# Optimization experiments

Hardware: AMD Instinct MI355X
Metric: run time of the kernel (lower is better)

## Reference

```python
import jax, jax.numpy as jnp
import numpy as np

N = 100000      # nodes per graph-batch
E = 1600000     # edges per graph-batch (avg degree 16)
G = 64          # graphs per batch (segments for mean pool)
DIN = 128
DH = 128


def setup_inputs() -> dict:
    key = jax.random.key(0)
    ks = jax.random.split(key, 14)
    x0 = jax.random.normal(ks[0], (N, DIN), jnp.float32)
    x1 = jax.random.normal(ks[1], (N, DIN), jnp.float32)
    edge_index0 = jax.random.randint(ks[2], (2, E), 0, N)
    edge_index1 = jax.random.randint(ks[3], (2, E), 0, N)
    batch0 = jnp.sort(jax.random.randint(ks[4], (N,), 0, G))
    batch1 = jnp.sort(jax.random.randint(ks[5], (N,), 0, G))
    s = 0.05
    W1 = jax.random.normal(ks[6], (DIN, DH), jnp.float32) * s
    b1 = jnp.zeros((DH,), jnp.float32)
    W2 = jax.random.normal(ks[7], (DH, DH), jnp.float32) * s
    b2 = jnp.zeros((DH,), jnp.float32)
    Wc1 = jax.random.normal(ks[8], (2 * DH, DH), jnp.float32) * s
    bc1 = jnp.zeros((DH,), jnp.float32)
    Wc2 = jax.random.normal(ks[9], (DH, 1), jnp.float32) * s
    bc2 = jnp.zeros((1,), jnp.float32)
    return dict(x0=x0, x1=x1, edge_index0=edge_index0, edge_index1=edge_index1,
                batch0=batch0, batch1=batch1,
                W1=W1, b1=b1, W2=W2, b2=b2, Wc1=Wc1, bc1=bc1, Wc2=Wc2, bc2=bc2)


def gcn_conv(x, edge_index, W, b):
    # PyG GCNConv: add self-loops, symmetric norm D^-1/2 (A+I) D^-1/2, then XW + b
    n = x.shape[0]
    sl = jnp.arange(n)
    src = jnp.concatenate([edge_index[0], sl])
    dst = jnp.concatenate([edge_index[1], sl])
    ones = jnp.ones(src.shape[0], x.dtype)
    deg = jax.ops.segment_sum(ones, dst, num_segments=n)
    dinv = jnp.where(deg > 0, jax.lax.rsqrt(deg), 0.0)
    norm = dinv[src] * dinv[dst]               # [E+N]
    h = x @ W                                   # [N, DH]
    msg = h[src] * norm[:, None]                # gather + scale
    return jax.ops.segment_sum(msg, dst, num_segments=n) + b


def graph_embedding(x, edge_index, batch, W1, b1, W2, b2):
    f = gcn_conv(x, edge_index, W1, b1)
    # dropout is identity in eval mode
    f = gcn_conv(f, edge_index, W2, b2)
    s = jax.ops.segment_sum(f, batch, num_segments=G)
    cnt = jax.ops.segment_sum(jnp.ones((f.shape[0],), f.dtype), batch, num_segments=G)
    return s / jnp.maximum(cnt, 1.0)[:, None]   # global_mean_pool -> [G, DH]


def reference(x0, x1, edge_index0, edge_index1, batch0, batch1,
              W1, b1, W2, b2, Wc1, bc1, Wc2, bc2):
    f0 = graph_embedding(x0, edge_index0, batch0, W1, b1, W2, b2)
    f1 = graph_embedding(x1, edge_index1, batch1, W1, b1, W2, b2)
    c = jnp.concatenate([f0, f1], axis=1)       # [G, 2*DH]
    h = jax.nn.sigmoid(c @ Wc1 + bc1)
    prob = jax.nn.sigmoid(h @ Wc2 + bc2)
    return prob[:, 0]                           # squeeze(-1) -> [G]
```

## Files before the change

kernel.cpp:

```cpp
#include <hip/hip_runtime.h>
#include <hip/hip_bf16.h>

#define NN 100000
#define NE 1600000
#define NG 64
#define DHID 128
#define PB 32
#define NBUCK 196
#define CAPE 10240
#define CHUNK 8192

#if __has_builtin(__builtin_amdgcn_cvt_pk_f32_fp8) && __has_builtin(__builtin_amdgcn_cvt_pk_fp8_f32)
#define FP8_HW 1
#endif

typedef float f32x2 __attribute__((ext_vector_type(2)));
typedef float f32x4 __attribute__((ext_vector_type(4)));
typedef short bf16x8 __attribute__((ext_vector_type(8)));

__device__ __forceinline__ float fp8_dec_sw(unsigned b) {
    unsigned u = ((b & 0x80u) << 24) | ((b & 0x7fu) << 20);
    return __uint_as_float(u) * 0x1p+120f;
}
__device__ __forceinline__ unsigned fp8_enc_sw(float f) {
    unsigned s = (__float_as_uint(f) >> 24) & 0x80u;
    float af = fabsf(f);
    if (!(af > 0x1p-10f)) return s;
    if (af > 448.f) af = 448.f;
    int e; float m = frexpf(af, &e);
    int ee = e + 6;
    unsigned bits;
    if (ee <= 0) {
        int k = (int)rintf(af * 512.0f);
        if (k > 7) k = 7;
        bits = (unsigned)k;
    } else {
        int mm = (int)rintf(m * 16.0f);
        if (mm == 16) { mm = 8; ee += 1; }
        if (ee > 15) { ee = 15; mm = 14; }
        bits = ((unsigned)ee << 3) | (unsigned)(mm - 8);
    }
    return s | bits;
}

__device__ __forceinline__ unsigned short fp8_pack2(float a, float b) {
#ifdef FP8_HW
    return (unsigned short)__builtin_amdgcn_cvt_pk_fp8_f32(a, b, 0, false);
#else
    return (unsigned short)(fp8_enc_sw(a) | (fp8_enc_sw(b) << 8));
#endif
}

__device__ __forceinline__ void fp8_acc4(unsigned u, float& a0, float& a1, float& a2, float& a3) {
#ifdef FP8_HW
    f32x2 lo = __builtin_amdgcn_cvt_pk_f32_fp8((int)u, false);
    f32x2 hi = __builtin_amdgcn_cvt_pk_f32_fp8((int)u, true);
    a0 += lo[0]; a1 += lo[1]; a2 += hi[0]; a3 += hi[1];
#else
    a0 += fp8_dec_sw(u & 0xffu);
    a1 += fp8_dec_sw((u >> 8) & 0xffu);
    a2 += fp8_dec_sw((u >> 16) & 0xffu);
    a3 += fp8_dec_sw(u >> 24);
#endif
}

__device__ __forceinline__ unsigned short f2bf(float f) {
    unsigned u = __float_as_uint(f);
    return (unsigned short)((u + 0x7FFFu + ((u >> 16) & 1u)) >> 16);
}


__global__ void initcur_kernel(int* __restrict__ cursor) {
    int t = threadIdx.x;
    if (t < NBUCK) cursor[t] = t * CAPE;
}

__global__ __launch_bounds__(256) void bin_kernel(const int* __restrict__ ei, int* __restrict__ cursor,
                                                  unsigned int* __restrict__ binned, int E) {
    __shared__ int hist[256], scn[256], lofs[256], lcur[256], basex[256];
    __shared__ unsigned int stage[CHUNK];
    __shared__ unsigned char stageB[CHUNK];
    int t = threadIdx.x;
    int c0 = blockIdx.x * CHUNK;
    int cend = min(c0 + CHUNK, E);
    hist[t] = 0;
    __syncthreads();
    for (int e = c0 + t; e < cend; e += 256)
        atomicAdd(&hist[((unsigned)ei[E + e]) >> 9], 1);
    __syncthreads();
    scn[t] = hist[t];
    __syncthreads();
    for (int off = 1; off < 256; off <<= 1) {
        int v = (t >= off) ? scn[t - off] : 0;
        __syncthreads();
        scn[t] += v;
        __syncthreads();
    }
    int excl = scn[t] - hist[t];
    lofs[t] = excl;
    lcur[t] = excl;
    if (hist[t] > 0) basex[t] = atomicAdd(&cursor[t], hist[t]);
    __syncthreads();
    for (int e = c0 + t; e < cend; e += 256) {
        int dst = ei[E + e], src = ei[e];
        int b = ((unsigned)dst) >> 9;
        int r = atomicAdd(&lcur[b], 1);
        stage[r]  = (((unsigned)(dst & 511)) << 17) | (unsigned)src;
        stageB[r] = (unsigned char)b;
    }
    __syncthreads();
    int cnt = cend - c0;
    for (int i = t; i < cnt; i += 256) {
        int b = stageB[i];
        binned[basex[b] + (i - lofs[b])] = stage[i];
    }
}

__global__ __launch_bounds__(256) void fine_kernel(const int* __restrict__ cursor,
                                                   unsigned int* __restrict__ binned,
                                                   float* __restrict__ dinv, int2* __restrict__ rng) {
    __shared__ unsigned int stage[CAPE];
    __shared__ int hist[512], ofs[512], lcur[512];
    __shared__ int pscan[256];
    int b = blockIdx.x, t = threadIdx.x;
    int gbase = b * CAPE;
    int cnt = min(cursor[b] - gbase, CAPE);
    for (int i = t; i < cnt; i += 256) stage[i] = binned[gbase + i];
    hist[t] = 0; hist[t + 256] = 0;
    __syncthreads();
    for (int i = t; i < cnt; i += 256) atomicAdd(&hist[stage[i] >> 17], 1);
    __syncthreads();
    int a0 = hist[2 * t], a1 = hist[2 * t + 1];
    pscan[t] = a0 + a1;
    __syncthreads();
    for (int off = 1; off < 256; off <<= 1) {
        int v = (t >= off) ? pscan[t - off] : 0;
        __syncthreads();
        pscan[t] += v;
        __syncthreads();
    }
    int pex = pscan[t] - (a0 + a1);
    ofs[2 * t] = pex;       ofs[2 * t + 1] = pex + a0;
    lcur[2 * t] = pex;      lcur[2 * t + 1] = pex + a0;
    __syncthreads();
#pragma unroll
    for (int q = 0; q < 2; ++q) {
        int l = t + 256 * q;
        int node = b * 512 + l;
        if (node < NN) {
            int dg = hist[l];
            dinv[node] = rsqrtf((float)(dg + 1));
            rng[node] = make_int2(gbase + ofs[l], gbase + ofs[l] + dg);
        }
    }
    for (int i = t; i < cnt; i += 256) {
        unsigned int p = stage[i];
        int l = p >> 17;
        int r = atomicAdd(&lcur[l], 1);
        binned[gbase + r] = p & 0x1FFFFu;
    }
}


__global__ void bounds_kernel(const int* __restrict__ b0, const int* __restrict__ b1,
                              int* __restrict__ bounds, int n) {
    int t = threadIdx.x;
    int gb = t >> 6, j = t & 63;
    const int* b = gb ? b1 : b0;
    int lo = 0, hi = n;
    while (lo < hi) { int mid = (lo + hi) >> 1; if (b[mid] < j) lo = mid + 1; else hi = mid; }
    bounds[gb * 65 + j] = lo;
    if (j == 0) bounds[gb * 65 + 64] = n;
}


__global__ __launch_bounds__(256) void wpack_kernel(const float* __restrict__ W, unsigned short* __restrict__ Wp) {
    for (int o = blockIdx.x * 256 + threadIdx.x; o < 128 * 128; o += 2048) {
        int j = o & 7, l = (o >> 3) & 63, tile = o >> 9;
        int kt = tile >> 3, ct = tile & 7;
        int k = kt * 32 + ((l >> 4) << 3) + j;
        int c = ct * 16 + (l & 15);
        Wp[o] = f2bf(W[k * 128 + c]);
    }
}


template<bool BF16IN>
__global__ __launch_bounds__(256) void gemm_mfma(const void* __restrict__ Avoid,
                                                 const unsigned short* __restrict__ Wp,
                                                 const float* __restrict__ dinv,
                                                 unsigned int* __restrict__ Hs8dw, int n) {
    int wave = threadIdx.x >> 6, lane = threadIdx.x & 63;
    int row_base = blockIdx.x * 64 + wave * 16;
    int r = lane & 15, kg = lane >> 4;
    int rowc = min(row_base + r, n - 1);

    bf16x8 af[4];
    if (BF16IN) {
        const uint4* A = (const uint4*)Avoid;
#pragma unroll
        for (int kt = 0; kt < 4; ++kt) {
            uint4 p = A[(size_t)rowc * 16 + kt * 4 + kg];
            af[kt] = *(bf16x8*)&p;
        }
    } else {
        const float4* A = (const float4*)Avoid;
#pragma unroll
        for (int kt = 0; kt < 4; ++kt) {
            float4 p0 = A[(size_t)rowc * 32 + kt * 8 + kg * 2];
            float4 p1 = A[(size_t)rowc * 32 + kt * 8 + kg * 2 + 1];
            bf16x8 a;
            a[0] = (short)f2bf(p0.x); a[1] = (short)f2bf(p0.y);
            a[2] = (short)f2bf(p0.z); a[3] = (short)f2bf(p0.w);
            a[4] = (short)f2bf(p1.x); a[5] = (short)f2bf(p1.y);
            a[6] = (short)f2bf(p1.z); a[7] = (short)f2bf(p1.w);
            af[kt] = a;
        }
    }

    f32x4 acc[8] = {};
    const bf16x8* Wf = (const bf16x8*)Wp;
#pragma unroll
    for (int kt = 0; kt < 4; ++kt) {
#pragma unroll
        for (int ct = 0; ct < 8; ++ct) {
            bf16x8 bf = Wf[(kt * 8 + ct) * 64 + lane];
            acc[ct] = __builtin_amdgcn_mfma_f32_16x16x32_bf16(af[kt], bf, acc[ct], 0, 0, 0);
        }
    }

    float dvr[4]; bool rok[4]; int erow[4];
#pragma unroll
    for (int reg = 0; reg < 4; ++reg) {
        erow[reg] = row_base + ((lane >> 4) << 2) + reg;
        rok[reg] = erow[reg] < n;
        dvr[reg] = dinv[min(erow[reg], n - 1)];
    }
#pragma unroll
    for (int ct = 0; ct < 8; ++ct) {
#pragma unroll
        for (int reg = 0; reg < 4; ++reg) {
            float v = acc[ct][reg] * dvr[reg];
            float v1 = __shfl_xor(v, 1);
            unsigned us = fp8_pack2(v, v1);
            unsigned u2 = (unsigned)__shfl_xor((int)us, 2);
            if ((lane & 3) == 0 && rok[reg]) {
                unsigned dword = (us & 0xffffu) | (u2 << 16);
                Hs8dw[(size_t)erow[reg] * 32 + ct * 4 + ((lane & 15) >> 2)] = dword;
            }
        }
    }
}


__global__ __launch_bounds__(256) void conv_gather(const unsigned int* __restrict__ Hs8,
                                                   const int2* __restrict__ rng,
                                                   const int* __restrict__ csr, const float* __restrict__ dinv,
                                                   const float* __restrict__ bias, uint2* __restrict__ out16, int n) {
    int wave = blockIdx.x * 4 + (threadIdx.x >> 6);
    int lane = threadIdx.x & 63;
    if (wave >= n) return;
    int d = wave;
    int half = lane >> 5;
    int h = lane & 31;
    int2 se = rng[d];
    int k0 = se.x, k1 = se.y;
    float a0 = 0.f, a1 = 0.f, a2 = 0.f, a3 = 0.f;
    int k = k0 + half;
    for (; k + 6 < k1; k += 8) {
        int s0 = csr[k], s1 = csr[k + 2], s2 = csr[k + 4], s3 = csr[k + 6];
        unsigned u0 = Hs8[(size_t)s0 * 32 + h];
        unsigned u1 = Hs8[(size_t)s1 * 32 + h];
        unsigned u2 = Hs8[(size_t)s2 * 32 + h];
        unsigned u3 = Hs8[(size_t)s3 * 32 + h];
        fp8_acc4(u0, a0, a1, a2, a3);
        fp8_acc4(u1, a0, a1, a2, a3);
        fp8_acc4(u2, a0, a1, a2, a3);
        fp8_acc4(u3, a0, a1, a2, a3);
    }
    for (; k < k1; k += 2) {
        unsigned u = Hs8[(size_t)csr[k] * 32 + h];
        fp8_acc4(u, a0, a1, a2, a3);
    }
    if (half == 0) {
        unsigned ud = Hs8[(size_t)d * 32 + h];
        fp8_acc4(ud, a0, a1, a2, a3);
    }
    a0 += __shfl_xor(a0, 32);
    a1 += __shfl_xor(a1, 32);
    a2 += __shfl_xor(a2, 32);
    a3 += __shfl_xor(a3, 32);
    if (half == 0) {
        float dv = dinv[d];
        float4 b = ((const float4*)bias)[h];
        unsigned short w0 = f2bf(fmaf(a0, dv, b.x));
        unsigned short w1 = f2bf(fmaf(a1, dv, b.y));
        unsigned short w2 = f2bf(fmaf(a2, dv, b.z));
        unsigned short w3 = f2bf(fmaf(a3, dv, b.w));
        uint2 o;
        o.x = (unsigned)w0 | ((unsigned)w1 << 16);
        o.y = (unsigned)w2 | ((unsigned)w3 << 16);
        out16[(size_t)d * 32 + h] = o;
    }
}


__global__ __launch_bounds__(256) void pool_part(const unsigned int* __restrict__ F16,
                                                 const int* __restrict__ bounds,
                                                 float* __restrict__ partial) {
    __shared__ float sh[512];
    int g   = blockIdx.x / PB;
    int sub = blockIdx.x % PB;
    int s = bounds[g], e = bounds[g + 1];
    int len = e - s;
    int chunk = (len + PB - 1) / PB;
    int is = s + sub * chunk;
    int ie = min(is + chunk, e);
    int cp = threadIdx.x & 63;
    int quarter = threadIdx.x >> 6;
    float acc0 = 0.f, acc1 = 0.f;
    for (int i = is + quarter; i < ie; i += 4) {
        unsigned u = F16[(size_t)i * 64 + cp];
        acc0 += __uint_as_float(u << 16);
        acc1 += __uint_as_float(u & 0xffff0000u);
    }
    sh[threadIdx.x] = acc0;
    sh[threadIdx.x + 256] = acc1;
    __syncthreads();
    if (threadIdx.x < 64) {
        float m0 = sh[cp] + sh[64 + cp] + sh[128 + cp] + sh[192 + cp];
        float m1 = sh[256 + cp] + sh[320 + cp] + sh[384 + cp] + sh[448 + cp];
        partial[((size_t)g * PB + sub) * 128 + 2 * cp]     = m0;
        partial[((size_t)g * PB + sub) * 128 + 2 * cp + 1] = m1;
    }
}


__global__ __launch_bounds__(128) void pool_finish(const float* __restrict__ partial, const int* __restrict__ bounds,
                                                   float* __restrict__ pool) {
    int gg = blockIdx.x;
    int gb = gg >> 6, g = gg & 63;
    int col = threadIdx.x;
    const float* p = partial + ((size_t)gb * NG + g) * PB * 128;
    float acc = 0.f;
#pragma unroll
    for (int sub = 0; sub < PB; ++sub) acc += p[sub * 128 + col];
    int len = bounds[gb * 65 + g + 1] - bounds[gb * 65 + g];
    pool[(size_t)gg * 128 + col] = acc / fmaxf((float)len, 1.0f);
}


__global__ __launch_bounds__(128) void classifier_kernel(const float* __restrict__ pool,
                                                         const float* __restrict__ Wc1, const float* __restrict__ bc1,
                                                         const float* __restrict__ Wc2, const float* __restrict__ bc2,
                                                         float* __restrict__ out) {
    __shared__ float sh[128];
    int g = blockIdx.x;
    int j = threadIdx.x;
    float acc = bc1[j];
    const float* p0 = pool + (size_t)g * 128;
    const float* p1 = pool + (size_t)(NG + g) * 128;
    for (int k = 0; k < 128; ++k) acc = fmaf(p0[k], Wc1[k * 128 + j], acc);
    for (int k = 0; k < 128; ++k) acc = fmaf(p1[k], Wc1[(128 + k) * 128 + j], acc);
    float h = 1.0f / (1.0f + expf(-acc));
    sh[j] = h * Wc2[j];
    __syncthreads();
    for (int off = 64; off > 0; off >>= 1) {
        if (j < off) sh[j] += sh[j + off];
        __syncthreads();
    }
    if (j == 0) out[g] = 1.0f / (1.0f + expf(-(sh[0] + bc2[0])));
}


extern "C" void kernel_launch(void* const* d_in, const int* in_sizes, int n_in,
                              void* d_out, int out_size, void* d_ws, size_t ws_size,
                              hipStream_t stream) {
    const float* x[2]     = {(const float*)d_in[0], (const float*)d_in[1]};
    const int*   ei[2]    = {(const int*)d_in[2], (const int*)d_in[3]};
    const int*   batch[2] = {(const int*)d_in[4], (const int*)d_in[5]};
    const float* W1  = (const float*)d_in[6];
    const float* b1  = (const float*)d_in[7];
    const float* W2  = (const float*)d_in[8];
    const float* b2  = (const float*)d_in[9];
    const float* Wc1 = (const float*)d_in[10];
    const float* bc1 = (const float*)d_in[11];
    const float* Wc2 = (const float*)d_in[12];
    const float* bc2 = (const float*)d_in[13];
    float* out = (float*)d_out;

    char* w = (char*)d_ws;
    unsigned short*  buf16  = (unsigned short*)w;  w += (size_t)NN * DHID * 2;
    unsigned short*  hs     = (unsigned short*)w;  w += (size_t)NN * DHID;
    unsigned int*    binned = (unsigned int*)w;    w += (size_t)NBUCK * CAPE * 4;
    int2*            rng    = (int2*)w;            w += (size_t)NN * 8;
    float*           dinv   = (float*)w;           w += (size_t)NN * 4;
    unsigned short*  wp1    = (unsigned short*)w;  w += (size_t)128 * 128 * 2;
    unsigned short*  wp2    = (unsigned short*)w;  w += (size_t)128 * 128 * 2;
    int*             cursor = (int*)w;             w += (size_t)NBUCK * 4 + 16;
    int*             bounds = (int*)w;             w += 2 * 65 * 4 + 8;
    float*           partial= (float*)w;           w += (size_t)2 * NG * PB * DHID * 4;
    float*           pool   = (float*)w;           w += (size_t)2 * NG * DHID * 4;

    if ((size_t)(w - (char*)d_ws) > ws_size) return;

    bounds_kernel<<<1, 128, 0, stream>>>(batch[0], batch[1], bounds, NN);
    wpack_kernel<<<8, 256, 0, stream>>>(W1, wp1);
    wpack_kernel<<<8, 256, 0, stream>>>(W2, wp2);

    const int gemm_grid = (NN + 63) / 64;

    for (int g = 0; g < 2; ++g) {
        initcur_kernel<<<1, 256, 0, stream>>>(cursor);
        bin_kernel<<<(NE + CHUNK - 1) / CHUNK, 256, 0, stream>>>(ei[g], cursor, binned, NE);
        fine_kernel<<<NBUCK, 256, 0, stream>>>(cursor, binned, dinv, rng);

        gemm_mfma<false><<<gemm_grid, 256, 0, stream>>>(x[g], wp1, dinv, (unsigned int*)hs, NN);
        conv_gather<<<(NN + 3) / 4, 256, 0, stream>>>((const unsigned int*)hs, rng, (const int*)binned, dinv, b1, (uint2*)buf16, NN);
        gemm_mfma<true><<<gemm_grid, 256, 0, stream>>>(buf16, wp2, dinv, (unsigned int*)hs, NN);
        conv_gather<<<(NN + 3) / 4, 256, 0, stream>>>((const unsigned int*)hs, rng, (const int*)binned, dinv, b2, (uint2*)buf16, NN);

        pool_part<<<NG * PB, 256, 0, stream>>>((const unsigned int*)buf16, bounds + g * 65, partial + (size_t)g * NG * PB * DHID);
    }

    pool_finish<<<2 * NG, 128, 0, stream>>>(partial, bounds, pool);
    classifier_kernel<<<NG, 128, 0, stream>>>(pool, Wc1, bc1, Wc2, bc2, out);
}
```

Baseline: 431.9 us.

## Split feature columns into quarter planes so gather working set fits cache

The fp8 H matrix and the bf16 activation buffer are stored as four column-quarter planes (32 features each). conv_gather now launches one grid slice per quarter and handles two nodes per wave, eight lanes per node, so each pass's random gathers touch a smaller plane. The aim is better L2/MALL hit rates on the random source-row loads. In exchange the CSR index is read four times, so the index loads are marked nontemporal. Smaller changes fold the two wpack launches into one, reset the cursor inside fine_kernel instead of relaunching initcur per graph, and adapt the GEMM and pool indexing to the new layout.

```diff
diff --git a/kernel.cpp b/kernel.cpp
--- a/kernel.cpp
+++ b/kernel.cpp
@@ -9,6 +9,7 @@
 #define NBUCK 196
 #define CAPE 10240
 #define CHUNK 8192
+#define QP 4
 
 #if __has_builtin(__builtin_amdgcn_cvt_pk_f32_fp8) && __has_builtin(__builtin_amdgcn_cvt_pk_fp8_f32)
 #define FP8_HW 1
@@ -116,7 +117,7 @@
     }
 }
 
-__global__ __launch_bounds__(256) void fine_kernel(const int* __restrict__ cursor,
+__global__ __launch_bounds__(256) void fine_kernel(int* __restrict__ cursor,
                                                    unsigned int* __restrict__ binned,
                                                    float* __restrict__ dinv, int2* __restrict__ rng) {
     __shared__ unsigned int stage[CAPE];
@@ -159,6 +160,7 @@
         int r = atomicAdd(&lcur[l], 1);
         binned[gbase + r] = p & 0x1FFFFu;
     }
+    if (t == 0) cursor[b] = gbase;
 }
 
 
@@ -174,14 +176,17 @@
 }
 
 
-__global__ __launch_bounds__(256) void wpack_kernel(const float* __restrict__ W, unsigned short* __restrict__ Wp) {
-    for (int o = blockIdx.x * 256 + threadIdx.x; o < 128 * 128; o += 2048) {
-        int j = o & 7, l = (o >> 3) & 63, tile = o >> 9;
-        int kt = tile >> 3, ct = tile & 7;
-        int k = kt * 32 + ((l >> 4) << 3) + j;
-        int c = ct * 16 + (l & 15);
-        Wp[o] = f2bf(W[k * 128 + c]);
-    }
+__global__ __launch_bounds__(256) void wpack_kernel(const float* __restrict__ W1, const float* __restrict__ W2,
+                                                    unsigned short* __restrict__ Wp1, unsigned short* __restrict__ Wp2) {
+    int o = blockIdx.x * 256 + threadIdx.x;
+    const float* W = (o < 16384) ? W1 : W2;
+    unsigned short* Wp = (o < 16384) ? Wp1 : Wp2;
+    int oo = o & 16383;
+    int j = oo & 7, l = (oo >> 3) & 63, tile = oo >> 9;
+    int kt = tile >> 3, ct = tile & 7;
+    int k = kt * 32 + ((l >> 4) << 3) + j;
+    int c = ct * 16 + (l & 15);
+    Wp[oo] = f2bf(W[k * 128 + c]);
 }
 
 
@@ -200,7 +205,7 @@
         const uint4* A = (const uint4*)Avoid;
 #pragma unroll
         for (int kt = 0; kt < 4; ++kt) {
-            uint4 p = A[(size_t)rowc * 16 + kt * 4 + kg];
+            uint4 p = A[((size_t)kt * n + rowc) * 4 + kg];
             af[kt] = *(bf16x8*)&p;
         }
     } else {
@@ -246,7 +251,7 @@
             unsigned u2 = (unsigned)__shfl_xor((int)us, 2);
             if ((lane & 3) == 0 && rok[reg]) {
                 unsigned dword = (us & 0xffffu) | (u2 << 16);
-                Hs8dw[(size_t)erow[reg] * 32 + ct * 4 + ((lane & 15) >> 2)] = dword;
+                Hs8dw[((size_t)(ct >> 1) * n + erow[reg]) * 8 + (ct & 1) * 4 + ((lane & 15) >> 2)] = dword;
             }
         }
     }
@@ -256,58 +261,59 @@
 __global__ __launch_bounds__(256) void conv_gather(const unsigned int* __restrict__ Hs8,
                                                    const int2* __restrict__ rng,
                                                    const int* __restrict__ csr, const float* __restrict__ dinv,
-                                                   const float* __restrict__ bias, uint2* __restrict__ out16, int n) {
-    int wave = blockIdx.x * 4 + (threadIdx.x >> 6);
+                                                   const float* __restrict__ bias,
+                                                   unsigned long long* __restrict__ out16,
+                                                   int n, int nblk) {
+    int q  = blockIdx.x / nblk;
+    int nb = blockIdx.x - q * nblk;
     int lane = threadIdx.x & 63;
-    if (wave >= n) return;
-    int d = wave;
     int half = lane >> 5;
-    int h = lane & 31;
+    int sub  = lane & 31;
+    int slot = sub >> 3;
+    int dw   = sub & 7;
+    int d = nb * 8 + (threadIdx.x >> 6) * 2 + half;
+    if (d >= n) return;
+    const unsigned int* Hq = Hs8 + (size_t)q * n * 8;
     int2 se = rng[d];
     int k0 = se.x, k1 = se.y;
     float a0 = 0.f, a1 = 0.f, a2 = 0.f, a3 = 0.f;
-    int k = k0 + half;
-    for (; k + 6 < k1; k += 8) {
-        int s0 = csr[k], s1 = csr[k + 2], s2 = csr[k + 4], s3 = csr[k + 6];
-        unsigned u0 = Hs8[(size_t)s0 * 32 + h];
-        unsigned u1 = Hs8[(size_t)s1 * 32 + h];
-        unsigned u2 = Hs8[(size_t)s2 * 32 + h];
-        unsigned u3 = Hs8[(size_t)s3 * 32 + h];
+    int k = k0 + slot;
+    for (; k + 4 < k1; k += 8) {
+        int s0 = __builtin_nontemporal_load(&csr[k]);
+        int s1 = __builtin_nontemporal_load(&csr[k + 4]);
+        unsigned u0 = Hq[(size_t)s0 * 8 + dw];
+        unsigned u1 = Hq[(size_t)s1 * 8 + dw];
         fp8_acc4(u0, a0, a1, a2, a3);
         fp8_acc4(u1, a0, a1, a2, a3);
-        fp8_acc4(u2, a0, a1, a2, a3);
-        fp8_acc4(u3, a0, a1, a2, a3);
-    }
-    for (; k < k1; k += 2) {
-        unsigned u = Hs8[(size_t)csr[k] * 32 + h];
+    }
+    for (; k < k1; k += 4) {
+        int s = __builtin_nontemporal_load(&csr[k]);
+        unsigned u = Hq[(size_t)s * 8 + dw];
         fp8_acc4(u, a0, a1, a2, a3);
     }
-    if (half == 0) {
-        unsigned ud = Hs8[(size_t)d * 32 + h];
+    if (slot == 0) {
+        unsigned ud = Hq[(size_t)d * 8 + dw];
         fp8_acc4(ud, a0, a1, a2, a3);
     }
-    a0 += __shfl_xor(a0, 32);
-    a1 += __shfl_xor(a1, 32);
-    a2 += __shfl_xor(a2, 32);
-    a3 += __shfl_xor(a3, 32);
-    if (half == 0) {
+    a0 += __shfl_xor(a0, 8);  a1 += __shfl_xor(a1, 8);  a2 += __shfl_xor(a2, 8);  a3 += __shfl_xor(a3, 8);
+    a0 += __shfl_xor(a0, 16); a1 += __shfl_xor(a1, 16); a2 += __shfl_xor(a2, 16); a3 += __shfl_xor(a3, 16);
+    if (slot == 0) {
         float dv = dinv[d];
-        float4 b = ((const float4*)bias)[h];
+        float4 b = ((const float4*)bias)[q * 8 + dw];
         unsigned short w0 = f2bf(fmaf(a0, dv, b.x));
         unsigned short w1 = f2bf(fmaf(a1, dv, b.y));
         unsigned short w2 = f2bf(fmaf(a2, dv, b.z));
         unsigned short w3 = f2bf(fmaf(a3, dv, b.w));
-        uint2 o;
-        o.x = (unsigned)w0 | ((unsigned)w1 << 16);
-        o.y = (unsigned)w2 | ((unsigned)w3 << 16);
-        out16[(size_t)d * 32 + h] = o;
+        unsigned long long o = (unsigned long long)((unsigned)w0 | ((unsigned)w1 << 16))
+                             | ((unsigned long long)((unsigned)w2 | ((unsigned)w3 << 16)) << 32);
+        __builtin_nontemporal_store(o, &out16[((size_t)q * n + d) * 8 + dw]);
     }
 }
 
 
 __global__ __launch_bounds__(256) void pool_part(const unsigned int* __restrict__ F16,
                                                  const int* __restrict__ bounds,
-                                                 float* __restrict__ partial) {
+                                                 float* __restrict__ partial, int n) {
     __shared__ float sh[512];
     int g   = blockIdx.x / PB;
     int sub = blockIdx.x % PB;
@@ -316,11 +322,12 @@
     int chunk = (len + PB - 1) / PB;
     int is = s + sub * chunk;
     int ie = min(is + chunk, e);
-    int cp = threadIdx.x & 63;
-    int quarter = threadIdx.x >> 6;
+    int cp  = threadIdx.x & 63;
+    int il  = threadIdx.x >> 6;
+    size_t qbase = (size_t)(cp >> 4) * n * 16 + (cp & 15);
     float acc0 = 0.f, acc1 = 0.f;
-    for (int i = is + quarter; i < ie; i += 4) {
-        unsigned u = F16[(size_t)i * 64 + cp];
+    for (int i = is + il; i < ie; i += 4) {
+        unsigned u = F16[qbase + (size_t)i * 16];
         acc0 += __uint_as_float(u << 16);
         acc1 += __uint_as_float(u & 0xffff0000u);
     }
@@ -405,22 +412,26 @@
     if ((size_t)(w - (char*)d_ws) > ws_size) return;
 
     bounds_kernel<<<1, 128, 0, stream>>>(batch[0], batch[1], bounds, NN);
-    wpack_kernel<<<8, 256, 0, stream>>>(W1, wp1);
-    wpack_kernel<<<8, 256, 0, stream>>>(W2, wp2);
+    wpack_kernel<<<128, 256, 0, stream>>>(W1, W2, wp1, wp2);
+    initcur_kernel<<<1, 256, 0, stream>>>(cursor);
 
     const int gemm_grid = (NN + 63) / 64;
+    const int conv_nblk = (NN + 7) / 8;
+    const int conv_grid = QP * conv_nblk;
 
     for (int g = 0; g < 2; ++g) {
-        initcur_kernel<<<1, 256, 0, stream>>>(cursor);
         bin_kernel<<<(NE + CHUNK - 1) / CHUNK, 256, 0, stream>>>(ei[g], cursor, binned, NE);
         fine_kernel<<<NBUCK, 256, 0, stream>>>(cursor, binned, dinv, rng);
 
         gemm_mfma<false><<<gemm_grid, 256, 0, stream>>>(x[g], wp1, dinv, (unsigned int*)hs, NN);
-        conv_gather<<<(NN + 3) / 4, 256, 0, stream>>>((const unsigned int*)hs, rng, (const int*)binned, dinv, b1, (uint2*)buf16, NN);
+        conv_gather<<<conv_grid, 256, 0, stream>>>((const unsigned int*)hs, rng, (const int*)binned, dinv, b1,
+                                                   (unsigned long long*)buf16, NN, conv_nblk);
         gemm_mfma<true><<<gemm_grid, 256, 0, stream>>>(buf16, wp2, dinv, (unsigned int*)hs, NN);
-        conv_gather<<<(NN + 3) / 4, 256, 0, stream>>>((const unsigned int*)hs, rng, (const int*)binned, dinv, b2, (uint2*)buf16, NN);
-
-        pool_part<<<NG * PB, 256, 0, stream>>>((const unsigned int*)buf16, bounds + g * 65, partial + (size_t)g * NG * PB * DHID);
+        conv_gather<<<conv_grid, 256, 0, stream>>>((const unsigned int*)hs, rng, (const int*)binned, dinv, b2,
+                                                   (unsigned long long*)buf16, NN, conv_nblk);
+
+        pool_part<<<NG * PB, 256, 0, stream>>>((const unsigned int*)buf16, bounds + g * 65,
+                                               partial + (size_t)g * NG * PB * DHID, NN);
     }
 
     pool_finish<<<2 * NG, 128, 0, stream>>>(partial, bounds, pool);
```

Measured after the change: 645.7 us. 49.5% more time.

## Batch edge binning for both graphs into single launches and unroll gather deeper

Applied to the files above, without the earlier changes.

Edge binning and CSR build for both graphs now run in one bin_kernel and one fine_kernel launch, each with a doubled grid, backed by doubled binned/rng/dinv buffers. This removes per-graph launch overhead and gives the GPU more blocks in flight. The two weight-pack launches are merged into one, and conv_gather gains a 16-edge unrolled loop so more independent gathers are outstanding. The cost is more workspace memory and more registers in the gather kernel, which could lower occupancy.

```diff
diff --git a/kernel.cpp b/kernel.cpp
--- a/kernel.cpp
+++ b/kernel.cpp
@@ -71,17 +71,22 @@
 
 
 __global__ void initcur_kernel(int* __restrict__ cursor) {
-    int t = threadIdx.x;
-    if (t < NBUCK) cursor[t] = t * CAPE;
-}
-
-__global__ __launch_bounds__(256) void bin_kernel(const int* __restrict__ ei, int* __restrict__ cursor,
-                                                  unsigned int* __restrict__ binned, int E) {
+    int i = blockIdx.x * 256 + threadIdx.x;
+    if (i < 2 * NBUCK) cursor[i] = i * CAPE;
+}
+
+__global__ __launch_bounds__(256) void bin_kernel(const int* __restrict__ ei0, const int* __restrict__ ei1,
+                                                  int* __restrict__ cursor,
+                                                  unsigned int* __restrict__ binned, int E, int nch) {
     __shared__ int hist[256], scn[256], lofs[256], lcur[256], basex[256];
     __shared__ unsigned int stage[CHUNK];
     __shared__ unsigned char stageB[CHUNK];
+    int g = blockIdx.x / nch;
+    int ch = blockIdx.x - g * nch;
+    const int* ei = g ? ei1 : ei0;
+    int* cur = cursor + g * NBUCK;
     int t = threadIdx.x;
-    int c0 = blockIdx.x * CHUNK;
+    int c0 = ch * CHUNK;
     int cend = min(c0 + CHUNK, E);
     hist[t] = 0;
     __syncthreads();
@@ -99,7 +104,7 @@
     int excl = scn[t] - hist[t];
     lofs[t] = excl;
     lcur[t] = excl;
-    if (hist[t] > 0) basex[t] = atomicAdd(&cursor[t], hist[t]);
+    if (hist[t] > 0) basex[t] = atomicAdd(&cur[t], hist[t]);
     __syncthreads();
     for (int e = c0 + t; e < cend; e += 256) {
         int dst = ei[E + e], src = ei[e];
@@ -116,15 +121,17 @@
     }
 }
 
-__global__ __launch_bounds__(256) void fine_kernel(const int* __restrict__ cursor,
+__global__ __launch_bounds__(256) void fine_kernel(int* __restrict__ cursor,
                                                    unsigned int* __restrict__ binned,
                                                    float* __restrict__ dinv, int2* __restrict__ rng) {
     __shared__ unsigned int stage[CAPE];
     __shared__ int hist[512], ofs[512], lcur[512];
     __shared__ int pscan[256];
-    int b = blockIdx.x, t = threadIdx.x;
-    int gbase = b * CAPE;
-    int cnt = min(cursor[b] - gbase, CAPE);
+    int bb = blockIdx.x;
+    int g = bb / NBUCK, bl = bb - g * NBUCK;
+    int t = threadIdx.x;
+    int gbase = bb * CAPE;
+    int cnt = min(cursor[bb] - gbase, CAPE);
     for (int i = t; i < cnt; i += 256) stage[i] = binned[gbase + i];
     hist[t] = 0; hist[t + 256] = 0;
     __syncthreads();
@@ -146,11 +153,11 @@
 #pragma unroll
     for (int q = 0; q < 2; ++q) {
         int l = t + 256 * q;
-        int node = b * 512 + l;
+        int node = bl * 512 + l;
         if (node < NN) {
             int dg = hist[l];
-            dinv[node] = rsqrtf((float)(dg + 1));
-            rng[node] = make_int2(gbase + ofs[l], gbase + ofs[l] + dg);
+            dinv[(size_t)g * NN + node] = rsqrtf((float)(dg + 1));
+            rng[(size_t)g * NN + node] = make_int2(gbase + ofs[l], gbase + ofs[l] + dg);
         }
     }
     for (int i = t; i < cnt; i += 256) {
@@ -159,6 +166,7 @@
         int r = atomicAdd(&lcur[l], 1);
         binned[gbase + r] = p & 0x1FFFFu;
     }
+    if (t == 0) cursor[bb] = gbase;
 }
 
 
@@ -174,14 +182,17 @@
 }
 
 
-__global__ __launch_bounds__(256) void wpack_kernel(const float* __restrict__ W, unsigned short* __restrict__ Wp) {
-    for (int o = blockIdx.x * 256 + threadIdx.x; o < 128 * 128; o += 2048) {
-        int j = o & 7, l = (o >> 3) & 63, tile = o >> 9;
-        int kt = tile >> 3, ct = tile & 7;
-        int k = kt * 32 + ((l >> 4) << 3) + j;
-        int c = ct * 16 + (l & 15);
-        Wp[o] = f2bf(W[k * 128 + c]);
-    }
+__global__ __launch_bounds__(256) void wpack_kernel(const float* __restrict__ W1, const float* __restrict__ W2,
+                                                    unsigned short* __restrict__ Wp1, unsigned short* __restrict__ Wp2) {
+    int o = blockIdx.x * 256 + threadIdx.x;
+    const float* W = (o < 16384) ? W1 : W2;
+    unsigned short* Wp = (o < 16384) ? Wp1 : Wp2;
+    int oo = o & 16383;
+    int j = oo & 7, l = (oo >> 3) & 63, tile = oo >> 9;
+    int kt = tile >> 3, ct = tile & 7;
+    int k = kt * 32 + ((l >> 4) << 3) + j;
+    int c = ct * 16 + (l & 15);
+    Wp[oo] = f2bf(W[k * 128 + c]);
 }
 
 
@@ -267,6 +278,26 @@
     int k0 = se.x, k1 = se.y;
     float a0 = 0.f, a1 = 0.f, a2 = 0.f, a3 = 0.f;
     int k = k0 + half;
+    for (; k + 14 < k1; k += 16) {
+        int s0 = csr[k],      s1 = csr[k + 2],  s2 = csr[k + 4],  s3 = csr[k + 6];
+        int s4 = csr[k + 8],  s5 = csr[k + 10], s6 = csr[k + 12], s7 = csr[k + 14];
+        unsigned u0 = Hs8[(size_t)s0 * 32 + h];
+        unsigned u1 = Hs8[(size_t)s1 * 32 + h];
+        unsigned u2 = Hs8[(size_t)s2 * 32 + h];
+        unsigned u3 = Hs8[(size_t)s3 * 32 + h];
+        unsigned u4 = Hs8[(size_t)s4 * 32 + h];
+        unsigned u5 = Hs8[(size_t)s5 * 32 + h];
+        unsigned u6 = Hs8[(size_t)s6 * 32 + h];
+        unsigned u7 = Hs8[(size_t)s7 * 32 + h];
+        fp8_acc4(u0, a0, a1, a2, a3);
+        fp8_acc4(u1, a0, a1, a2, a3);
+        fp8_acc4(u2, a0, a1, a2, a3);
+        fp8_acc4(u3, a0, a1, a2, a3);
+        fp8_acc4(u4, a0, a1, a2, a3);
+        fp8_acc4(u5, a0, a1, a2, a3);
+        fp8_acc4(u6, a0, a1, a2, a3);
+        fp8_acc4(u7, a0, a1, a2, a3);
+    }
     for (; k + 6 < k1; k += 8) {
         int s0 = csr[k], s1 = csr[k + 2], s2 = csr[k + 4], s3 = csr[k + 6];
         unsigned u0 = Hs8[(size_t)s0 * 32 + h];
@@ -392,33 +423,37 @@
     char* w = (char*)d_ws;
     unsigned short*  buf16  = (unsigned short*)w;  w += (size_t)NN * DHID * 2;
     unsigned short*  hs     = (unsigned short*)w;  w += (size_t)NN * DHID;
-    unsigned int*    binned = (unsigned int*)w;    w += (size_t)NBUCK * CAPE * 4;
-    int2*            rng    = (int2*)w;            w += (size_t)NN * 8;
-    float*           dinv   = (float*)w;           w += (size_t)NN * 4;
+    unsigned int*    binned = (unsigned int*)w;    w += (size_t)2 * NBUCK * CAPE * 4;
+    int2*            rng    = (int2*)w;            w += (size_t)2 * NN * 8;
+    float*           dinv   = (float*)w;           w += (size_t)2 * NN * 4;
     unsigned short*  wp1    = (unsigned short*)w;  w += (size_t)128 * 128 * 2;
     unsigned short*  wp2    = (unsigned short*)w;  w += (size_t)128 * 128 * 2;
-    int*             cursor = (int*)w;             w += (size_t)NBUCK * 4 + 16;
+    int*             cursor = (int*)w;             w += (size_t)2 * NBUCK * 4 + 16;
     int*             bounds = (int*)w;             w += 2 * 65 * 4 + 8;
     float*           partial= (float*)w;           w += (size_t)2 * NG * PB * DHID * 4;
     float*           pool   = (float*)w;           w += (size_t)2 * NG * DHID * 4;
 
     if ((size_t)(w - (char*)d_ws) > ws_size) return;
 
+    const int nch = (NE + CHUNK - 1) / CHUNK;
+
     bounds_kernel<<<1, 128, 0, stream>>>(batch[0], batch[1], bounds, NN);
-    wpack_kernel<<<8, 256, 0, stream>>>(W1, wp1);
-    wpack_kernel<<<8, 256, 0, stream>>>(W2, wp2);
+    wpack_kernel<<<128, 256, 0, stream>>>(W1, W2, wp1, wp2);
+    initcur_kernel<<<2, 256, 0, stream>>>(cursor);
+
+    bin_kernel<<<2 * nch, 256, 0, stream>>>(ei[0], ei[1], cursor, binned, NE, nch);
+    fine_kernel<<<2 * NBUCK, 256, 0, stream>>>(cursor, binned, dinv, rng);
 
     const int gemm_grid = (NN + 63) / 64;
 
     for (int g = 0; g < 2; ++g) {
-        initcur_kernel<<<1, 256, 0, stream>>>(cursor);
-        bin_kernel<<<(NE + CHUNK - 1) / CHUNK, 256, 0, stream>>>(ei[g], cursor, binned, NE);
-        fine_kernel<<<NBUCK, 256, 0, stream>>>(cursor, binned, dinv, rng);
-
-        gemm_mfma<false><<<gemm_grid, 256, 0, stream>>>(x[g], wp1, dinv, (unsigned int*)hs, NN);
-        conv_gather<<<(NN + 3) / 4, 256, 0, stream>>>((const unsigned int*)hs, rng, (const int*)binned, dinv, b1, (uint2*)buf16, NN);
-        gemm_mfma<true><<<gemm_grid, 256, 0, stream>>>(buf16, wp2, dinv, (unsigned int*)hs, NN);
-        conv_gather<<<(NN + 3) / 4, 256, 0, stream>>>((const unsigned int*)hs, rng, (const int*)binned, dinv, b2, (uint2*)buf16, NN);
+        const float* dv = dinv + (size_t)g * NN;
+        const int2*  rg = rng + (size_t)g * NN;
+
+        gemm_mfma<false><<<gemm_grid, 256, 0, stream>>>(x[g], wp1, dv, (unsigned int*)hs, NN);
+        conv_gather<<<(NN + 3) / 4, 256, 0, stream>>>((const unsigned int*)hs, rg, (const int*)binned, dv, b1, (uint2*)buf16, NN);
+        gemm_mfma<true><<<gemm_grid, 256, 0, stream>>>(buf16, wp2, dv, (unsigned int*)hs, NN);
+        conv_gather<<<(NN + 3) / 4, 256, 0, stream>>>((const unsigned int*)hs, rg, (const int*)binned, dv, b2, (uint2*)buf16, NN);
 
         pool_part<<<NG * PB, 256, 0, stream>>>((const unsigned int*)buf16, bounds + g * 65, partial + (size_t)g * NG * PB * DHID);
     }
```

Measured after the change: 387.3 us. 10.3% less time.
